# Performance work log

Measured on AMD Instinct MI355X. Metric: run time of the kernel, lower is better.

The kernel has to match this reference:

```python
import jax, jax.numpy as jnp
import numpy as np
import math

H = 2048
NH = 16
NKV = 4
HD = H // NH  # 128
N_REP = NH // NKV
EPS = 1e-6


def rms_norm(x, w, eps=1e-6):
    x32 = x.astype(jnp.float32)
    y = x32 * jax.lax.rsqrt(jnp.mean(x32 * x32, axis=-1, keepdims=True) + eps)
    return (y * w.astype(jnp.float32)).astype(x.dtype)


def mha(normed, key_in, val_in, q_w, k_w, v_w, o_w, bias):
    # normed: [b,s,H]; key_in/val_in: [b,n,H]; bias broadcastable to [b,nh,s,n]
    b, s, _ = normed.shape
    n = key_in.shape[1]
    q = (normed @ q_w).reshape(b, s, NH, HD).transpose(0, 2, 1, 3)      # [b,nh,s,d]
    k = (key_in @ k_w).reshape(b, n, NKV, HD).transpose(0, 2, 1, 3)     # [b,nkv,n,d]
    v = (val_in @ v_w).reshape(b, n, NKV, HD).transpose(0, 2, 1, 3)
    k = jnp.repeat(k, N_REP, axis=1)  # GQA expand -> [b,nh,n,d]
    v = jnp.repeat(v, N_REP, axis=1)
    scores = jnp.einsum('bhsd,bhnd->bhsn', q, k) / math.sqrt(HD) + bias
    probs = jax.nn.softmax(scores.astype(jnp.float32), axis=-1).astype(q.dtype)
    out = jnp.einsum('bhsn,bhnd->bhsd', probs, v)
    out = out.transpose(0, 2, 1, 3).reshape(b, s, NH * HD) @ o_w
    return out, probs


def setup_inputs() -> dict:
    key = jax.random.key(0)
    ks = jax.random.split(key, 20)
    B, S, ND, T = 2, 2048, 64, 2048
    w = lambda k, sh: (jax.random.normal(k, sh, dtype=jnp.float32) * 0.02)
    return {
        'hidden_states': jax.random.normal(ks[0], (B, S, H), dtype=jnp.float32),
        'doc_summary_key': jax.random.normal(ks[1], (B, ND, H), dtype=jnp.float32),
        'doc_summary_value': jax.random.normal(ks[2], (B, ND, H), dtype=jnp.float32),
        'doc_summary_mask': jnp.ones((B, ND), dtype=jnp.float32),
        'token_key': jax.random.normal(ks[3], (B, T, H), dtype=jnp.float32),
        'token_value': jax.random.normal(ks[4], (B, T, H), dtype=jnp.float32),
        'token_mask': jnp.ones((B, T), dtype=jnp.float32),
        'cn_w': jnp.ones((H,), dtype=jnp.float32),
        'cq_w': w(ks[5], (H, NH * HD)),
        'ck_w': w(ks[6], (H, NKV * HD)),
        'cv_w': w(ks[7], (H, NKV * HD)),
        'co_w': w(ks[8], (NH * HD, H)),
        'c_gate': jnp.array([-1.0], dtype=jnp.float32),
        'fn_w': jnp.ones((H,), dtype=jnp.float32),
        'fq_w': w(ks[9], (H, NH * HD)),
        'fk_w': w(ks[10], (H, NKV * HD)),
        'fv_w': w(ks[11], (H, NKV * HD)),
        'fo_w': w(ks[12], (NH * HD, H)),
        'f_gate': jnp.array([-1.0], dtype=jnp.float32),
        'doc_token_map': jax.random.randint(ks[13], (B, T), 0, ND, dtype=jnp.int64)
            if jax.config.jax_enable_x64 else jax.random.randint(ks[13], (B, T), 0, ND).astype(jnp.int32),
    }


def reference(hidden_states, doc_summary_key, doc_summary_value, doc_summary_mask,
              token_key, token_value, token_mask,
              cn_w, cq_w, ck_w, cv_w, co_w, c_gate,
              fn_w, fq_w, fk_w, fv_w, fo_w, f_gate,
              doc_token_map):
    # ---- coarse stage: cross-attention over document summaries ----
    normed = rms_norm(hidden_states, cn_w)
    coarse_bias = ((1.0 - doc_summary_mask) * -1e9)[:, None, None, :]  # [b,1,1,nd]
    attn_out, probs = mha(normed, doc_summary_key, doc_summary_value,
                          cq_w, ck_w, cv_w, co_w, coarse_bias)
    doc_scores = probs.mean(axis=(1, 2))  # [b,nd] avg over heads+query positions
    gate_c = jax.nn.sigmoid(c_gate).astype(attn_out.dtype)
    out = hidden_states + gate_c * attn_out

    # ---- fine stage: cross-attention over token KV with log-doc-score bias ----
    log_ds = jnp.log(doc_scores + EPS)
    doc_bias = jnp.take_along_axis(log_ds, doc_token_map, axis=1)  # [b,T]
    pad_bias = (1.0 - token_mask) * -1e9
    fine_bias = (doc_bias + pad_bias)[:, None, None, :]  # [b,1,1,T]
    normed_f = rms_norm(out, fn_w)
    attn_out_f, _ = mha(normed_f, token_key, token_value,
                        fq_w, fk_w, fv_w, fo_w, fine_bias)
    gate_f = jax.nn.sigmoid(f_gate).astype(attn_out_f.dtype)
    final = out + gate_f * attn_out_f
    return final
```

## Files before the change

### kernel.cpp

```cpp
#include <hip/hip_runtime.h>
#include <hip/hip_bf16.h>

typedef unsigned short u16;
typedef unsigned int u32;
typedef __attribute__((ext_vector_type(8))) short bf16x8;
typedef __attribute__((ext_vector_type(4))) float f32x4;

constexpr int NH = 16;
constexpr int H = 2048;
constexpr float SCALE = 0.08838834764831845f;
constexpr float L2E = 1.4426950408889634f;
constexpr float SCALE2 = SCALE * L2E;
constexpr float THR2 = 8.0f * L2E;

__device__ __forceinline__ u16 f2bf(float f) {
    u32 u = __float_as_uint(f);
    u32 r = u + 0x7fffu + ((u >> 16) & 1u);
    return (u16)(r >> 16);
}
__device__ __forceinline__ u32 pack2(float x, float y) {
    return (u32)f2bf(x) | ((u32)f2bf(y) << 16);
}
__device__ __forceinline__ u32 pack2_cvt(float x, float y) {
    __hip_bfloat162 h = __float22bfloat162_rn(float2{x, y});
    return *reinterpret_cast<u32*>(&h);
}

#define GLD_LDS16(gsrc, ldst)                                                  \
    __builtin_amdgcn_global_load_lds(                                          \
        (const __attribute__((address_space(1))) void*)(gsrc),                 \
        (__attribute__((address_space(3))) void*)(ldst), 16, 0, 0)

__global__ __launch_bounds__(256) void cvt_f32_bf16_2(const float* __restrict__ a,
                                                      u16* __restrict__ oa,
                                                      const float* __restrict__ b,
                                                      u16* __restrict__ ob, int n4) {
    int i = blockIdx.x * 256 + threadIdx.x;
    const float* in;
    u16* out;
    if (i < n4) { in = a; out = oa; }
    else if (i < 2 * n4) { i -= n4; in = b; out = ob; }
    else return;
    float4 v = reinterpret_cast<const float4*>(in)[i];
    uint2 o;
    o.x = pack2(v.x, v.y);
    o.y = pack2(v.z, v.w);
    reinterpret_cast<uint2*>(out)[i] = o;
}

__global__ __launch_bounds__(256)
void transpose_cvt4(const float* __restrict__ i0, const float* __restrict__ i1,
                    const float* __restrict__ i2, const float* __restrict__ i3,
                    u16* __restrict__ o0, u16* __restrict__ o1,
                    u16* __restrict__ o2, u16* __restrict__ o3, int K, int N) {
    const float* in = (blockIdx.z == 0) ? i0 : (blockIdx.z == 1) ? i1
                    : (blockIdx.z == 2) ? i2 : i3;
    u16* out = (blockIdx.z == 0) ? o0 : (blockIdx.z == 1) ? o1
             : (blockIdx.z == 2) ? o2 : o3;
    __shared__ u16 tile[32][33];
    int bn = blockIdx.x * 32, bk = blockIdx.y * 32;
    int tx = threadIdx.x & 31, ty = threadIdx.x >> 5;
#pragma unroll
    for (int r = 0; r < 32; r += 8)
        tile[tx][r + ty] = f2bf(in[(size_t)(bk + r + ty) * N + bn + tx]);
    __syncthreads();
#pragma unroll
    for (int r = 0; r < 32; r += 8)
        out[(size_t)(bn + r + ty) * K + bk + tx] = tile[r + ty][tx];
}

__global__ __launch_bounds__(256) void rmsnorm_kernel(const float* __restrict__ x,
                                                      const float* __restrict__ w,
                                                      u16* __restrict__ y) {
    int r = blockIdx.x;
    const float4* xr = reinterpret_cast<const float4*>(x + (size_t)r * H);
    int t = threadIdx.x;
    float4 v0 = xr[t * 2], v1 = xr[t * 2 + 1];
    float ss = v0.x * v0.x + v0.y * v0.y + v0.z * v0.z + v0.w * v0.w
             + v1.x * v1.x + v1.y * v1.y + v1.z * v1.z + v1.w * v1.w;
#pragma unroll
    for (int d = 1; d < 64; d <<= 1) ss += __shfl_xor(ss, d);
    __shared__ float red[4];
    if ((t & 63) == 0) red[t >> 6] = ss;
    __syncthreads();
    float tot = red[0] + red[1] + red[2] + red[3];
    float rs = rsqrtf(tot * (1.0f / H) + 1e-6f);
    const float4* wr = reinterpret_cast<const float4*>(w);
    float4 w0 = wr[t * 2], w1 = wr[t * 2 + 1];
    uint4 o;
    o.x = pack2(v0.x * rs * w0.x, v0.y * rs * w0.y);
    o.y = pack2(v0.z * rs * w0.z, v0.w * rs * w0.w);
    o.z = pack2(v1.x * rs * w1.x, v1.y * rs * w1.y);
    o.w = pack2(v1.z * rs * w1.z, v1.w * rs * w1.w);
    reinterpret_cast<uint4*>(y + (size_t)r * H)[t] = o;
}

template <int MODE, int BN>
__device__ __forceinline__
void gemm_body(const u16* __restrict__ A, const u16* __restrict__ Bt,
               u16* __restrict__ Cb, float* __restrict__ Cf,
               const float* __restrict__ resid, const float* __restrict__ gate_p,
               int N, int K, int brow, int bcol) {
    constexpr int WN = BN / 32;
    constexpr int BWROWS = BN / 4;
    __shared__ u16 As[2][128 * 64];
    __shared__ u16 Bs[2][BN * 64];
    const int t = threadIdx.x;
    const int lane = t & 63, wid = t >> 6;
    const int wm = wid >> 1, wn = wid & 1;
    const int l15 = lane & 15, hi = lane >> 4;
    const int rsw = l15 & 7;

    f32x4 acc[4][WN] = {};
    const int srow = lane >> 3;
    const int sseg = ((lane & 7) ^ srow) * 8;
    const u16* aBase = A + (size_t)(brow + wid * 32 + srow) * K + sseg;
    const u16* bBase = Bt + (size_t)(bcol + wid * BWROWS + srow) * K + sseg;

#define GSTAGE(KT, BF)                                                          \
    do {                                                                        \
        _Pragma("unroll")                                                       \
        for (int u = 0; u < 4; ++u)                                             \
            GLD_LDS16(aBase + (size_t)(u * 8) * K + (KT),                       \
                      &As[BF][(wid * 32 + u * 8) * 64]);                        \
        _Pragma("unroll")                                                       \
        for (int u = 0; u < BWROWS / 8; ++u)                                    \
            GLD_LDS16(bBase + (size_t)(u * 8) * K + (KT),                       \
                      &Bs[BF][(wid * BWROWS + u * 8) * 64]);                    \
    } while (0)

    GSTAGE(0, 0);
    __syncthreads();
    int buf = 0;
    for (int kt = 0; kt < K; kt += 64) {
        if (kt + 64 < K) GSTAGE(kt + 64, buf ^ 1);
        bf16x8 af[4][2], bfr[WN][2];
#pragma unroll
        for (int i = 0; i < 4; ++i) {
            int row = wm * 64 + i * 16 + l15;
#pragma unroll
            for (int ko = 0; ko < 2; ++ko)
                af[i][ko] = *reinterpret_cast<const bf16x8*>(
                    &As[buf][row * 64 + (((ko * 4 + hi) ^ rsw) * 8)]);
        }
#pragma unroll
        for (int j = 0; j < WN; ++j) {
            int row = wn * (BN / 2) + j * 16 + l15;
#pragma unroll
            for (int ko = 0; ko < 2; ++ko)
                bfr[j][ko] = *reinterpret_cast<const bf16x8*>(
                    &Bs[buf][row * 64 + (((ko * 4 + hi) ^ rsw) * 8)]);
        }
#pragma unroll
        for (int ko = 0; ko < 2; ++ko)
#pragma unroll
            for (int i = 0; i < 4; ++i)
#pragma unroll
                for (int j = 0; j < WN; ++j)
                    acc[i][j] = __builtin_amdgcn_mfma_f32_16x16x32_bf16(
                        af[i][ko], bfr[j][ko], acc[i][j], 0, 0, 0);
        __syncthreads();
        buf ^= 1;
    }
#undef GSTAGE

    float g = 0.f;
    if (MODE == 1) g = 1.0f / (1.0f + expf(-gate_p[0]));
    const int r0 = hi * 4, c0 = l15;
#pragma unroll
    for (int i = 0; i < 4; ++i) {
#pragma unroll
        for (int j = 0; j < WN; ++j) {
            int col = bcol + wn * (BN / 2) + j * 16 + c0;
#pragma unroll
            for (int r = 0; r < 4; ++r) {
                int row = brow + wm * 64 + i * 16 + r0 + r;
                float v = acc[i][j][r];
                if (MODE == 0) Cb[(size_t)row * N + col] = f2bf(v);
                else Cf[(size_t)row * N + col] = resid[(size_t)row * N + col] + g * v;
            }
        }
    }
}

template <int MODE, int BN>
__global__ __launch_bounds__(256)
void gemm_tn(const u16* __restrict__ A, const u16* __restrict__ Bt,
             u16* __restrict__ Cb, float* __restrict__ Cf,
             const float* __restrict__ resid, const float* __restrict__ gate_p,
             int M, int N, int K) {
    int nbx = gridDim.x;
    int nwg = nbx * gridDim.y;
    int lin = blockIdx.y * nbx + blockIdx.x;
    if (!(nwg & 7)) { int q = nwg >> 3; lin = (lin & 7) * q + (lin >> 3); }
    gemm_body<MODE, BN>(A, Bt, Cb, Cf, resid, gate_p, N, K,
                        (lin / nbx) * 128, (lin % nbx) * BN);
}

template <int MODE, int BN>
__global__ __launch_bounds__(256)
void gemm_tn_cvt(const u16* __restrict__ A, const u16* __restrict__ Bt,
                 u16* __restrict__ Cb, float* __restrict__ Cf,
                 const float* __restrict__ resid, const float* __restrict__ gate_p,
                 int M, int N, int K,
                 const float* __restrict__ ca, u16* __restrict__ coa,
                 const float* __restrict__ cb2, u16* __restrict__ cob, int n4) {
    if (blockIdx.z == 1) {
        int nblk = gridDim.x * gridDim.y;
        int stride = nblk * 256;
        for (int i = (blockIdx.y * gridDim.x + blockIdx.x) * 256 + threadIdx.x;
             i < 2 * n4; i += stride) {
            const float* in;
            u16* out;
            int j = i;
            if (j < n4) { in = ca; out = coa; }
            else { j -= n4; in = cb2; out = cob; }
            float4 v = reinterpret_cast<const float4*>(in)[j];
            uint2 o;
            o.x = pack2(v.x, v.y);
            o.y = pack2(v.z, v.w);
            reinterpret_cast<uint2*>(out)[j] = o;
        }
        return;
    }
    int nbx = gridDim.x;
    int nwg = nbx * gridDim.y;
    int lin = blockIdx.y * nbx + blockIdx.x;
    if (!(nwg & 7)) { int q = nwg >> 3; lin = (lin & 7) * q + (lin >> 3); }
    gemm_body<MODE, BN>(A, Bt, Cb, Cf, resid, gate_p, N, K,
                        (lin / nbx) * 128, (lin % nbx) * BN);
}

template <int MODE, int BN>
__global__ __launch_bounds__(256)
void gemm_tn_z2(const u16* __restrict__ A0, const u16* __restrict__ B0, u16* __restrict__ C0,
                const u16* __restrict__ A1, const u16* __restrict__ B1, u16* __restrict__ C1,
                int N, int K) {
    const u16* A = blockIdx.z ? A1 : A0;
    const u16* B = blockIdx.z ? B1 : B0;
    u16* C = blockIdx.z ? C1 : C0;
    gemm_body<MODE, BN>(A, B, C, nullptr, nullptr, nullptr, N, K,
                        blockIdx.y * 128, blockIdx.x * BN);
}

template <int MODE, int BN>
__global__ __launch_bounds__(256)
void gemm_tn_dual(const u16* __restrict__ A0, const u16* __restrict__ B0,
                  u16* __restrict__ C0, int N0, int nbx0,
                  const u16* __restrict__ A1, const u16* __restrict__ B1,
                  u16* __restrict__ C1, int N1, int nbx1, int K) {
    int lin = blockIdx.x;
    if (blockIdx.z == 0)
        gemm_body<MODE, BN>(A0, B0, C0, nullptr, nullptr, nullptr, N0, K,
                            (lin / nbx0) * 128, (lin % nbx0) * BN);
    else
        gemm_body<MODE, BN>(A1, B1, C1, nullptr, nullptr, nullptr, N1, K,
                            (lin / nbx1) * 128, (lin % nbx1) * BN);
}

__global__ __launch_bounds__(256)
void coarse_attn(const u16* __restrict__ q, const u16* __restrict__ kc,
                 const u16* __restrict__ vc, const float* __restrict__ mask,
                 float* __restrict__ doc_part, u16* __restrict__ attn_c) {
    constexpr int SC = 2048 / 64;
    int bid = blockIdx.x;
    int b = bid / (NH * SC);
    int rem = bid % (NH * SC);
    int h = rem / SC, sc = rem % SC;
    int kv = h >> 2;
    int t = threadIdx.x, lane = t & 63, wid = t >> 6;
    const int l15 = lane & 15, k0 = (lane >> 4) * 8;

    __shared__ u16 Kt[64 * 136];
    __shared__ u16 Vt[128 * 72];
    __shared__ u16 Pt[4][16 * 72];
    __shared__ float p_acc[64];

    {
        int n = t >> 2, s2 = t & 3;
        const u16* src = kc + (size_t)(b * 64 + n) * 512 + kv * 128;
#pragma unroll
        for (int u = 0; u < 4; ++u) {
            int sg = s2 + u * 4;
            *reinterpret_cast<uint4*>(&Kt[n * 136 + sg * 8]) =
                *reinterpret_cast<const uint4*>(src + sg * 8);
        }
    }
    {
        int n = t & 63, dblk = t >> 6;
        const u16* src = vc + (size_t)(b * 64 + n) * 512 + kv * 128 + dblk * 32;
#pragma unroll
        for (int u = 0; u < 4; ++u) {
            u16 tmp[8];
            *reinterpret_cast<uint4*>(tmp) = *reinterpret_cast<const uint4*>(src + u * 8);
#pragma unroll
            for (int e = 0; e < 8; ++e) Vt[(dblk * 32 + u * 8 + e) * 72 + n] = tmp[e];
        }
    }
    if (t < 64) p_acc[t] = 0.f;
    __syncthreads();

    int qrow = sc * 64 + wid * 16 + l15;
    const u16* qsrc = q + (size_t)(b * 2048 + qrow) * 2048 + h * 128;
    bf16x8 af[4];
#pragma unroll
    for (int kk = 0; kk < 4; ++kk)
        af[kk] = *reinterpret_cast<const bf16x8*>(qsrc + kk * 32 + k0);

    f32x4 sc4[4] = {};
#pragma unroll
    for (int kk = 0; kk < 4; ++kk)
#pragma unroll
        for (int j = 0; j < 4; ++j) {
            bf16x8 bfr = *reinterpret_cast<const bf16x8*>(&Kt[(j * 16 + l15) * 136 + kk * 32 + k0]);
            sc4[j] = __builtin_amdgcn_mfma_f32_16x16x32_bf16(af[kk], bfr, sc4[j], 0, 0, 0);
        }

    float s[4][4];
#pragma unroll
    for (int j = 0; j < 4; ++j) {
        float bia = (1.0f - mask[b * 64 + j * 16 + l15]) * (-1e9f * L2E);
#pragma unroll
        for (int r = 0; r < 4; ++r) s[j][r] = sc4[j][r] * SCALE2 + bia;
    }
    float m4[4], l4[4];
#pragma unroll
    for (int r = 0; r < 4; ++r) {
        float m = fmaxf(fmaxf(s[0][r], s[1][r]), fmaxf(s[2][r], s[3][r]));
#pragma unroll
        for (int d = 1; d < 16; d <<= 1) m = fmaxf(m, __shfl_xor(m, d));
        m4[r] = m;
    }
#pragma unroll
    for (int r = 0; r < 4; ++r) {
        float l = 0.f;
#pragma unroll
        for (int j = 0; j < 4; ++j) { s[j][r] = exp2f(s[j][r] - m4[r]); l += s[j][r]; }
#pragma unroll
        for (int d = 1; d < 16; d <<= 1) l += __shfl_xor(l, d);
        l4[r] = l;
    }
#pragma unroll
    for (int j = 0; j < 4; ++j) {
        float cs = 0.f;
#pragma unroll
        for (int r = 0; r < 4; ++r) {
            float pr = s[j][r] / l4[r];
            Pt[wid][((lane >> 4) * 4 + r) * 72 + j * 16 + l15] = f2bf(pr);
            cs += pr;
        }
        cs += __shfl_xor(cs, 16);
        cs += __shfl_xor(cs, 32);
        if (lane < 16) atomicAdd(&p_acc[j * 16 + lane], cs);
    }
    __syncthreads();

    f32x4 o4[8] = {};
#pragma unroll
    for (int kk2 = 0; kk2 < 2; ++kk2) {
        bf16x8 a2 = *reinterpret_cast<const bf16x8*>(&Pt[wid][l15 * 72 + kk2 * 32 + k0]);
#pragma unroll
        for (int j2 = 0; j2 < 8; ++j2) {
            bf16x8 b2 = *reinterpret_cast<const bf16x8*>(&Vt[(j2 * 16 + l15) * 72 + kk2 * 32 + k0]);
            o4[j2] = __builtin_amdgcn_mfma_f32_16x16x32_bf16(a2, b2, o4[j2], 0, 0, 0);
        }
    }
#pragma unroll
    for (int j2 = 0; j2 < 8; ++j2)
#pragma unroll
        for (int r = 0; r < 4; ++r) {
            int row = sc * 64 + wid * 16 + (lane >> 4) * 4 + r;
            attn_c[(size_t)(b * 2048 + row) * 2048 + h * 128 + j2 * 16 + l15] = f2bf(o4[j2][r]);
        }
    if (t < 64) atomicAdd(&doc_part[(blockIdx.x & 7) * 128 + b * 64 + t], p_acc[t]);
}

__global__ __launch_bounds__(256)
void bias_kernel(const float* __restrict__ doc_part, const int* __restrict__ map,
                 const float* __restrict__ tmask, float* __restrict__ bias) {
    __shared__ float lg[128];
    int t = threadIdx.x;
    if (t < 128) {
        float s = 0.f;
#pragma unroll
        for (int i = 0; i < 8; ++i) s += doc_part[i * 128 + t];
        lg[t] = logf(s / 32768.0f + 1e-6f);
    }
    __syncthreads();
    int i = blockIdx.x * 256 + t;
    if (i >= 2 * 2048) return;
    int b = i >> 11;
    bias[i] = (lg[b * 64 + map[i]] + (1.0f - tmask[i]) * -1e9f) * L2E;
}

__global__ __launch_bounds__(256, 2)
void flash_attn(const u16* __restrict__ q, const u16* __restrict__ kf,
                const u16* __restrict__ vT, const float* __restrict__ bias,
                u16* __restrict__ attn_f) {
    int bid = blockIdx.x;
    int b = bid >> 8;
    int rem = bid & 255;
    int h = rem >> 4, sc = rem & 15;
    int kv = h >> 2;
    int t = threadIdx.x, lane = t & 63, wid = t >> 6;
    const int l15 = lane & 15, hi = lane >> 4;
    const int k0 = hi * 8;
    const int rswp = l15 & 7;

    __shared__ u16 Kt[2][64 * 128];
    __shared__ u16 Vt[2][128 * 64];
    __shared__ u16 Pt[4][32 * 64];

    bf16x8 qf4[2][4];
#pragma unroll
    for (int f = 0; f < 2; ++f) {
        int qrow = sc * 128 + wid * 32 + f * 16 + l15;
        const u16* qsrc = q + (size_t)(b * 2048 + qrow) * 2048 + h * 128;
#pragma unroll
        for (int kk = 0; kk < 4; ++kk)
            qf4[f][kk] = *reinterpret_cast<const bf16x8*>(qsrc + kk * 32 + k0);
    }

    const int krl = lane >> 4, kslot = lane & 15;
    const int vrl = lane >> 3, vslot = lane & 7;
    const u16* kbase = kf + (size_t)(b * 2048) * 512 + kv * 128;
    const u16* vbase = vT + (size_t)(kv * 128) * 4096 + b * 2048;
    const float* bbase = bias + b * 2048;

#define STAGE_K(TT, BF)                                                            \
    do {                                                                           \
        _Pragma("unroll")                                                          \
        for (int u = 0; u < 4; ++u) {                                              \
            int row = wid * 16 + u * 4 + krl;                                      \
            const u16* src = kbase + (size_t)((TT) + row) * 512                    \
                             + ((kslot ^ (row & 7)) * 8);                          \
            GLD_LDS16(src, &Kt[BF][(wid * 16 + u * 4) * 128]);                     \
        }                                                                          \
    } while (0)
#define STAGE_V(TT, BF)                                                            \
    do {                                                                           \
        _Pragma("unroll")                                                          \
        for (int u = 0; u < 4; ++u) {                                              \
            int row = wid * 32 + u * 8 + vrl;                                      \
            const u16* src = vbase + (size_t)row * 4096 + (TT)                     \
                             + ((vslot ^ (row & 7)) * 8);                          \
            GLD_LDS16(src, &Vt[BF][(wid * 32 + u * 8) * 64]);                      \
        }                                                                          \
    } while (0)

    float mstate[2] = {-1e30f, -1e30f}, lstate[2] = {0.f, 0.f};
    f32x4 o4[2][8] = {};

    STAGE_K(0, 0);
    STAGE_V(0, 0);
    __syncthreads();
    int par = 0;

    for (int t0 = 0; t0 < 2048; t0 += 64) {
        int t1 = (t0 + 64) & 2047;
        STAGE_K(t1, par ^ 1);
        STAGE_V(t1, par ^ 1);

        f32x4 st0[4] = {}, st1[4] = {};
        __builtin_amdgcn_s_setprio(1);
#pragma unroll
        for (int kk = 0; kk < 4; ++kk)
#pragma unroll
            for (int kb = 0; kb < 4; ++kb) {
                int row = kb * 16 + l15;
                bf16x8 kfrag = *reinterpret_cast<const bf16x8*>(
                    &Kt[par][row * 128 + (((kk * 4 + hi) ^ (row & 7)) * 8)]);
                st0[kb] = __builtin_amdgcn_mfma_f32_16x16x32_bf16(kfrag, qf4[0][kk], st0[kb], 0, 0, 0);
                st1[kb] = __builtin_amdgcn_mfma_f32_16x16x32_bf16(kfrag, qf4[1][kk], st1[kb], 0, 0, 0);
            }
        __builtin_amdgcn_s_setprio(0);

        float p[2][4][4];
        float pmax[2] = {-1e30f, -1e30f};
#pragma unroll
        for (int kb = 0; kb < 4; ++kb) {
            float4 b4 = *reinterpret_cast<const float4*>(bbase + t0 + kb * 16 + hi * 4);
            float bb[4] = {b4.x, b4.y, b4.z, b4.w};
#pragma unroll
            for (int r = 0; r < 4; ++r) {
                float v0 = st0[kb][r] * SCALE2 + bb[r];
                float v1 = st1[kb][r] * SCALE2 + bb[r];
                p[0][kb][r] = v0;
                p[1][kb][r] = v1;
                pmax[0] = fmaxf(pmax[0], v0);
                pmax[1] = fmaxf(pmax[1], v1);
            }
        }
#pragma unroll
        for (int f = 0; f < 2; ++f) {
            pmax[f] = fmaxf(pmax[f], __shfl_xor(pmax[f], 16));
            pmax[f] = fmaxf(pmax[f], __shfl_xor(pmax[f], 32));
        }

        bool need = (pmax[0] > mstate[0] + THR2) || (pmax[1] > mstate[1] + THR2);
        if (__any(need)) {
#pragma unroll
            for (int f = 0; f < 2; ++f) {
                float mnew = fmaxf(mstate[f], pmax[f]);
                float sco = exp2f(mstate[f] - mnew);
                float sco_out[4];
#pragma unroll
                for (int r = 0; r < 4; ++r) sco_out[r] = __shfl(sco, hi * 4 + r);
#pragma unroll
                for (int j2 = 0; j2 < 8; ++j2)
#pragma unroll
                    for (int r = 0; r < 4; ++r) o4[f][j2][r] *= sco_out[r];
                lstate[f] *= sco;
                mstate[f] = mnew;
            }
        }

#pragma unroll
        for (int f = 0; f < 2; ++f) {
            float lt = 0.f;
#pragma unroll
            for (int kb = 0; kb < 4; ++kb)
#pragma unroll
                for (int r = 0; r < 4; ++r) {
                    p[f][kb][r] = exp2f(p[f][kb][r] - mstate[f]);
                    lt += p[f][kb][r];
                }
            lt += __shfl_xor(lt, 16);
            lt += __shfl_xor(lt, 32);
            lstate[f] += lt;
        }

#pragma unroll
        for (int f = 0; f < 2; ++f)
#pragma unroll
            for (int kb = 0; kb < 4; ++kb) {
                uint2 w;
                w.x = pack2_cvt(p[f][kb][0], p[f][kb][1]);
                w.y = pack2_cvt(p[f][kb][2], p[f][kb][3]);
                int idx = (f * 16 + l15) * 64
                        + (((kb * 2 + (hi >> 1)) ^ rswp) * 8) + (hi & 1) * 4;
                *reinterpret_cast<uint2*>(&Pt[wid][idx]) = w;
            }

        __builtin_amdgcn_s_setprio(1);
#pragma unroll
        for (int kc2 = 0; kc2 < 2; ++kc2) {
            bf16x8 pa0 = *reinterpret_cast<const bf16x8*>(
                &Pt[wid][l15 * 64 + (((kc2 * 4 + hi) ^ rswp) * 8)]);
            bf16x8 pa1 = *reinterpret_cast<const bf16x8*>(
                &Pt[wid][(16 + l15) * 64 + (((kc2 * 4 + hi) ^ rswp) * 8)]);
#pragma unroll
            for (int j2 = 0; j2 < 8; ++j2) {
                int d = j2 * 16 + l15;
                bf16x8 vb = *reinterpret_cast<const bf16x8*>(
                    &Vt[par][d * 64 + (((kc2 * 4 + hi) ^ (d & 7)) * 8)]);
                o4[0][j2] = __builtin_amdgcn_mfma_f32_16x16x32_bf16(pa0, vb, o4[0][j2], 0, 0, 0);
                o4[1][j2] = __builtin_amdgcn_mfma_f32_16x16x32_bf16(pa1, vb, o4[1][j2], 0, 0, 0);
            }
        }
        __builtin_amdgcn_s_setprio(0);
        __syncthreads();
        par ^= 1;
    }
#undef STAGE_K
#undef STAGE_V

#pragma unroll
    for (int f = 0; f < 2; ++f) {
        float linv[4];
#pragma unroll
        for (int r = 0; r < 4; ++r) linv[r] = 1.0f / __shfl(lstate[f], hi * 4 + r);
#pragma unroll
        for (int j2 = 0; j2 < 8; ++j2)
#pragma unroll
            for (int r = 0; r < 4; ++r) {
                int row = sc * 128 + wid * 32 + f * 16 + hi * 4 + r;
                attn_f[(size_t)(b * 2048 + row) * 2048 + h * 128 + j2 * 16 + l15] =
                    f2bf(o4[f][j2][r] * linv[r]);
            }
    }
}

extern "C" void kernel_launch(void* const* d_in, const int* in_sizes, int n_in,
                              void* d_out, int out_size, void* d_ws, size_t ws_size,
                              hipStream_t stream) {
    const float* hidden = (const float*)d_in[0];
    const float* dsk    = (const float*)d_in[1];
    const float* dsv    = (const float*)d_in[2];
    const float* dsmask = (const float*)d_in[3];
    const float* tk     = (const float*)d_in[4];
    const float* tv     = (const float*)d_in[5];
    const float* tmask  = (const float*)d_in[6];
    const float* cn_w   = (const float*)d_in[7];
    const float* cq_w   = (const float*)d_in[8];
    const float* ck_w   = (const float*)d_in[9];
    const float* cv_w   = (const float*)d_in[10];
    const float* co_w   = (const float*)d_in[11];
    const float* c_gate = (const float*)d_in[12];
    const float* fn_w   = (const float*)d_in[13];
    const float* fq_w   = (const float*)d_in[14];
    const float* fk_w   = (const float*)d_in[15];
    const float* fv_w   = (const float*)d_in[16];
    const float* fo_w   = (const float*)d_in[17];
    const float* f_gate = (const float*)d_in[18];
    const int*   map    = (const int*)d_in[19];
    float* out_f = (float*)d_out;

    char* ws = (char*)d_ws;
    size_t off = 0;
    auto alloc = [&](size_t bytes) {
        char* p = ws + off;
        off += (bytes + 255) & ~(size_t)255;
        return p;
    };
    u16*  normA = (u16*)alloc(4096ULL * 2048 * 2);
    u16*  qbuf  = (u16*)alloc(4096ULL * 2048 * 2);
    u16*  kc    = (u16*)alloc(128ULL * 512 * 2);
    u16*  vc    = (u16*)alloc(128ULL * 512 * 2);
    u16*  kfb   = (u16*)alloc(4096ULL * 512 * 2);
    u16*  vTb   = (u16*)alloc(512ULL * 4096 * 2);
    u16*  tkb   = (u16*)alloc(4096ULL * 2048 * 2);
    u16*  tvb   = (u16*)alloc(4096ULL * 2048 * 2);
    u16*  dskb  = (u16*)alloc(128ULL * 2048 * 2);
    u16*  dsvb  = (u16*)alloc(128ULL * 2048 * 2);
    u16*  cqT   = (u16*)alloc(2048ULL * 2048 * 2);
    u16*  ckT   = (u16*)alloc(512ULL * 2048 * 2);
    u16*  cvT   = (u16*)alloc(512ULL * 2048 * 2);
    u16*  coT   = (u16*)alloc(2048ULL * 2048 * 2);
    u16*  fqT   = (u16*)alloc(2048ULL * 2048 * 2);
    u16*  fkT   = (u16*)alloc(512ULL * 2048 * 2);
    u16*  fvT   = (u16*)alloc(512ULL * 2048 * 2);
    u16*  foT   = (u16*)alloc(2048ULL * 2048 * 2);
    float* doc_part = (float*)alloc(8 * 128 * 4);
    float* biasb    = (float*)alloc(4096 * 4);

    hipMemsetAsync(doc_part, 0, 8 * 128 * 4, stream);

    transpose_cvt4<<<dim3(64, 64, 4), 256, 0, stream>>>(cq_w, co_w, fq_w, fo_w,
                                                        cqT, coT, fqT, foT, 2048, 2048);
    transpose_cvt4<<<dim3(16, 64, 4), 256, 0, stream>>>(ck_w, cv_w, fk_w, fv_w,
                                                        ckT, cvT, fkT, fvT, 2048, 512);

    cvt_f32_bf16_2<<<(2 * 128 * 2048 / 4 + 255) / 256, 256, 0, stream>>>(
        dsk, dskb, dsv, dsvb, 128 * 2048 / 4);
    rmsnorm_kernel<<<4096, 256, 0, stream>>>(hidden, cn_w, normA);

    gemm_tn_cvt<0, 128><<<dim3(16, 32, 2), 256, 0, stream>>>(
        normA, cqT, qbuf, nullptr, nullptr, nullptr, 4096, 2048, 2048,
        tk, tkb, tv, tvb, 4096 * 2048 / 4);
    gemm_tn_z2<0, 64><<<dim3(8, 1, 2), 256, 0, stream>>>(dskb, ckT, kc, dsvb, cvT, vc, 512, 2048);

    coarse_attn<<<1024, 256, 0, stream>>>(qbuf, kc, vc, dsmask, doc_part, normA);
    bias_kernel<<<16, 256, 0, stream>>>(doc_part, map, tmask, biasb);

    gemm_tn<1, 128><<<dim3(16, 32), 256, 0, stream>>>(normA, coT, nullptr, out_f, hidden, c_gate, 4096, 2048, 2048);

    rmsnorm_kernel<<<4096, 256, 0, stream>>>(out_f, fn_w, qbuf);
    gemm_tn<0, 128><<<dim3(16, 32), 256, 0, stream>>>(qbuf, fqT, normA, nullptr, nullptr, nullptr, 4096, 2048, 2048);
    gemm_tn_dual<0, 64><<<dim3(256, 1, 2), 256, 0, stream>>>(
        tkb, fkT, kfb, 512, 8,
        fvT, tvb, vTb, 4096, 64, 2048);

    flash_attn<<<512, 256, 0, stream>>>(normA, kfb, vTb, biasb, qbuf);

    gemm_tn<1, 128><<<dim3(16, 32), 256, 0, stream>>>(qbuf, foT, nullptr, out_f, out_f, f_gate, 4096, 2048, 2048);
}
```

Before: 432.8 us.

## Merge fine Q/K/V projection GEMMs into one launch and fuse cvt into rmsnorm

Result: faster. 414.3 us, median of 2 (-4.3%).

```diff
diff --git a/kernel.cpp b/kernel.cpp
--- a/kernel.cpp
+++ b/kernel.cpp
@@ -30,23 +30,6 @@
     __builtin_amdgcn_global_load_lds(                                          \
         (const __attribute__((address_space(1))) void*)(gsrc),                 \
         (__attribute__((address_space(3))) void*)(ldst), 16, 0, 0)
-
-__global__ __launch_bounds__(256) void cvt_f32_bf16_2(const float* __restrict__ a,
-                                                      u16* __restrict__ oa,
-                                                      const float* __restrict__ b,
-                                                      u16* __restrict__ ob, int n4) {
-    int i = blockIdx.x * 256 + threadIdx.x;
-    const float* in;
-    u16* out;
-    if (i < n4) { in = a; out = oa; }
-    else if (i < 2 * n4) { i -= n4; in = b; out = ob; }
-    else return;
-    float4 v = reinterpret_cast<const float4*>(in)[i];
-    uint2 o;
-    o.x = pack2(v.x, v.y);
-    o.y = pack2(v.z, v.w);
-    reinterpret_cast<uint2*>(out)[i] = o;
-}
 
 __global__ __launch_bounds__(256)
 void transpose_cvt4(const float* __restrict__ i0, const float* __restrict__ i1,
@@ -69,12 +52,32 @@
         out[(size_t)(bn + r + ty) * K + bk + tx] = tile[r + ty][tx];
 }
 
-__global__ __launch_bounds__(256) void rmsnorm_kernel(const float* __restrict__ x,
-                                                      const float* __restrict__ w,
-                                                      u16* __restrict__ y) {
-    int r = blockIdx.x;
+__global__ __launch_bounds__(256)
+void rmsnorm_cvt(const float* __restrict__ x, const float* __restrict__ w,
+                 u16* __restrict__ y, int nrows,
+                 const float* __restrict__ ca, u16* __restrict__ coa,
+                 const float* __restrict__ cb, u16* __restrict__ cob, int n4) {
+    int blk = blockIdx.x;
+    int t = threadIdx.x;
+    if (blk >= nrows) {
+        int nb = gridDim.x - nrows;
+        int stride = nb * 256;
+        for (int i = (blk - nrows) * 256 + t; i < 2 * n4; i += stride) {
+            const float* in;
+            u16* out;
+            int j = i;
+            if (j < n4) { in = ca; out = coa; }
+            else { j -= n4; in = cb; out = cob; }
+            float4 v = reinterpret_cast<const float4*>(in)[j];
+            uint2 o;
+            o.x = pack2(v.x, v.y);
+            o.y = pack2(v.z, v.w);
+            reinterpret_cast<uint2*>(out)[j] = o;
+        }
+        return;
+    }
+    int r = blk;
     const float4* xr = reinterpret_cast<const float4*>(x + (size_t)r * H);
-    int t = threadIdx.x;
     float4 v0 = xr[t * 2], v1 = xr[t * 2 + 1];
     float ss = v0.x * v0.x + v0.y * v0.y + v0.z * v0.z + v0.w * v0.w
              + v1.x * v1.x + v1.y * v1.y + v1.z * v1.z + v1.w * v1.w;
@@ -97,14 +100,15 @@
 
 template <int MODE, int BN>
 __device__ __forceinline__
-void gemm_body(const u16* __restrict__ A, const u16* __restrict__ Bt,
+void gemm_body(u16* __restrict__ smem,
+               const u16* __restrict__ A, const u16* __restrict__ Bt,
                u16* __restrict__ Cb, float* __restrict__ Cf,
                const float* __restrict__ resid, const float* __restrict__ gate_p,
                int N, int K, int brow, int bcol) {
     constexpr int WN = BN / 32;
     constexpr int BWROWS = BN / 4;
-    __shared__ u16 As[2][128 * 64];
-    __shared__ u16 Bs[2][BN * 64];
+    u16* Asb = smem;
+    u16* Bsb = smem + 2 * 128 * 64;
     const int t = threadIdx.x;
     const int lane = t & 63, wid = t >> 6;
     const int wm = wid >> 1, wn = wid & 1;
@@ -122,11 +126,11 @@
         _Pragma("unroll")                                                       \
         for (int u = 0; u < 4; ++u)                                             \
             GLD_LDS16(aBase + (size_t)(u * 8) * K + (KT),                       \
-                      &As[BF][(wid * 32 + u * 8) * 64]);                        \
+                      Asb + (BF) * 8192 + (wid * 32 + u * 8) * 64);             \
         _Pragma("unroll")                                                       \
         for (int u = 0; u < BWROWS / 8; ++u)                                    \
             GLD_LDS16(bBase + (size_t)(u * 8) * K + (KT),                       \
-                      &Bs[BF][(wid * BWROWS + u * 8) * 64]);                    \
+                      Bsb + (BF) * (BN * 64) + (wid * BWROWS + u * 8) * 64);    \
     } while (0)
 
     GSTAGE(0, 0);
@@ -134,6 +138,8 @@
     int buf = 0;
     for (int kt = 0; kt < K; kt += 64) {
         if (kt + 64 < K) GSTAGE(kt + 64, buf ^ 1);
+        const u16* as = Asb + buf * 8192;
+        const u16* bs = Bsb + buf * (BN * 64);
         bf16x8 af[4][2], bfr[WN][2];
 #pragma unroll
         for (int i = 0; i < 4; ++i) {
@@ -141,7 +147,7 @@
 #pragma unroll
             for (int ko = 0; ko < 2; ++ko)
                 af[i][ko] = *reinterpret_cast<const bf16x8*>(
-                    &As[buf][row * 64 + (((ko * 4 + hi) ^ rsw) * 8)]);
+                    &as[row * 64 + (((ko * 4 + hi) ^ rsw) * 8)]);
         }
 #pragma unroll
         for (int j = 0; j < WN; ++j) {
@@ -149,7 +155,7 @@
 #pragma unroll
             for (int ko = 0; ko < 2; ++ko)
                 bfr[j][ko] = *reinterpret_cast<const bf16x8*>(
-                    &Bs[buf][row * 64 + (((ko * 4 + hi) ^ rsw) * 8)]);
+                    &bs[row * 64 + (((ko * 4 + hi) ^ rsw) * 8)]);
         }
 #pragma unroll
         for (int ko = 0; ko < 2; ++ko)
@@ -189,11 +195,12 @@
              u16* __restrict__ Cb, float* __restrict__ Cf,
              const float* __restrict__ resid, const float* __restrict__ gate_p,
              int M, int N, int K) {
+    __shared__ u16 smem[16384 + BN * 128];
     int nbx = gridDim.x;
     int nwg = nbx * gridDim.y;
     int lin = blockIdx.y * nbx + blockIdx.x;
     if (!(nwg & 7)) { int q = nwg >> 3; lin = (lin & 7) * q + (lin >> 3); }
-    gemm_body<MODE, BN>(A, Bt, Cb, Cf, resid, gate_p, N, K,
+    gemm_body<MODE, BN>(smem, A, Bt, Cb, Cf, resid, gate_p, N, K,
                         (lin / nbx) * 128, (lin % nbx) * BN);
 }
 
@@ -205,6 +212,7 @@
                  int M, int N, int K,
                  const float* __restrict__ ca, u16* __restrict__ coa,
                  const float* __restrict__ cb2, u16* __restrict__ cob, int n4) {
+    __shared__ u16 smem[16384 + BN * 128];
     if (blockIdx.z == 1) {
         int nblk = gridDim.x * gridDim.y;
         int stride = nblk * 256;
@@ -227,7 +235,7 @@
     int nwg = nbx * gridDim.y;
     int lin = blockIdx.y * nbx + blockIdx.x;
     if (!(nwg & 7)) { int q = nwg >> 3; lin = (lin & 7) * q + (lin >> 3); }
-    gemm_body<MODE, BN>(A, Bt, Cb, Cf, resid, gate_p, N, K,
+    gemm_body<MODE, BN>(smem, A, Bt, Cb, Cf, resid, gate_p, N, K,
                         (lin / nbx) * 128, (lin % nbx) * BN);
 }
 
@@ -236,26 +244,44 @@
 void gemm_tn_z2(const u16* __restrict__ A0, const u16* __restrict__ B0, u16* __restrict__ C0,
                 const u16* __restrict__ A1, const u16* __restrict__ B1, u16* __restrict__ C1,
                 int N, int K) {
+    __shared__ u16 smem[16384 + BN * 128];
     const u16* A = blockIdx.z ? A1 : A0;
     const u16* B = blockIdx.z ? B1 : B0;
     u16* C = blockIdx.z ? C1 : C0;
-    gemm_body<MODE, BN>(A, B, C, nullptr, nullptr, nullptr, N, K,
+    gemm_body<MODE, BN>(smem, A, B, C, nullptr, nullptr, nullptr, N, K,
                         blockIdx.y * 128, blockIdx.x * BN);
 }
 
-template <int MODE, int BN>
-__global__ __launch_bounds__(256)
-void gemm_tn_dual(const u16* __restrict__ A0, const u16* __restrict__ B0,
-                  u16* __restrict__ C0, int N0, int nbx0,
-                  const u16* __restrict__ A1, const u16* __restrict__ B1,
-                  u16* __restrict__ C1, int N1, int nbx1, int K) {
+__global__ __launch_bounds__(256)
+void gemm_triple(const u16* __restrict__ Aq, const u16* __restrict__ Bq,
+                 u16* __restrict__ Cq,
+                 const u16* __restrict__ Ak, const u16* __restrict__ Bk,
+                 u16* __restrict__ Ck,
+                 const u16* __restrict__ Av, const u16* __restrict__ Bv,
+                 u16* __restrict__ Cv, int K) {
+    __shared__ u16 smem[32768];
     int lin = blockIdx.x;
-    if (blockIdx.z == 0)
-        gemm_body<MODE, BN>(A0, B0, C0, nullptr, nullptr, nullptr, N0, K,
-                            (lin / nbx0) * 128, (lin % nbx0) * BN);
-    else
-        gemm_body<MODE, BN>(A1, B1, C1, nullptr, nullptr, nullptr, N1, K,
-                            (lin / nbx1) * 128, (lin % nbx1) * BN);
+    if (!(lin & 1)) {
+        int l = lin >> 1;
+        int q = 512 >> 3;
+        l = (l & 7) * q + (l >> 3);
+        gemm_body<0, 128>(smem, Aq, Bq, Cq, nullptr, nullptr, nullptr, 2048, K,
+                          (l / 16) * 128, (l % 16) * 128);
+    } else {
+        int j = lin >> 1;
+        if (j < 256) {
+            int q = 256 >> 3;
+            j = (j & 7) * q + (j >> 3);
+            gemm_body<0, 64>(smem, Ak, Bk, Ck, nullptr, nullptr, nullptr, 512, K,
+                             (j / 8) * 128, (j % 8) * 64);
+        } else {
+            j -= 256;
+            int q = 256 >> 3;
+            j = (j & 7) * q + (j >> 3);
+            gemm_body<0, 64>(smem, Av, Bv, Cv, nullptr, nullptr, nullptr, 4096, K,
+                             (j / 64) * 128, (j % 64) * 64);
+        }
+    }
 }
 
 __global__ __launch_bounds__(256)
@@ -641,9 +667,8 @@
     transpose_cvt4<<<dim3(16, 64, 4), 256, 0, stream>>>(ck_w, cv_w, fk_w, fv_w,
                                                         ckT, cvT, fkT, fvT, 2048, 512);
 
-    cvt_f32_bf16_2<<<(2 * 128 * 2048 / 4 + 255) / 256, 256, 0, stream>>>(
-        dsk, dskb, dsv, dsvb, 128 * 2048 / 4);
-    rmsnorm_kernel<<<4096, 256, 0, stream>>>(hidden, cn_w, normA);
+    rmsnorm_cvt<<<4096 + 256, 256, 0, stream>>>(hidden, cn_w, normA, 4096,
+                                                dsk, dskb, dsv, dsvb, 128 * 2048 / 4);
 
     gemm_tn_cvt<0, 128><<<dim3(16, 32, 2), 256, 0, stream>>>(
         normA, cqT, qbuf, nullptr, nullptr, nullptr, 4096, 2048, 2048,
@@ -655,11 +680,11 @@
 
     gemm_tn<1, 128><<<dim3(16, 32), 256, 0, stream>>>(normA, coT, nullptr, out_f, hidden, c_gate, 4096, 2048, 2048);
 
-    rmsnorm_kernel<<<4096, 256, 0, stream>>>(out_f, fn_w, qbuf);
-    gemm_tn<0, 128><<<dim3(16, 32), 256, 0, stream>>>(qbuf, fqT, normA, nullptr, nullptr, nullptr, 4096, 2048, 2048);
-    gemm_tn_dual<0, 64><<<dim3(256, 1, 2), 256, 0, stream>>>(
-        tkb, fkT, kfb, 512, 8,
-        fvT, tvb, vTb, 4096, 64, 2048);
+    rmsnorm_cvt<<<4096, 256, 0, stream>>>(out_f, fn_w, qbuf, 4096,
+                                          nullptr, nullptr, nullptr, nullptr, 0);
+    gemm_triple<<<1024, 256, 0, stream>>>(qbuf, fqT, normA,
+                                          tkb, fkT, kfb,
+                                          fvT, tvb, vTb, 2048);
 
     flash_attn<<<512, 256, 0, stream>>>(normA, kfb, vTb, biasb, qbuf);
 
```
